# Optimization experiments

Measured on AMD Instinct MI355X. Metric: run time of the kernel, lower is better.

The kernel has to match this reference:

```python
import jax, jax.numpy as jnp
import numpy as np
from jax import lax

B, T, D_IN, H, OUT = 64, 500, 89, 512, 61


def setup_inputs() -> dict:
    key = jax.random.key(0)
    ks = jax.random.split(key, 12)
    s = lambda *sh: 1.0 / np.sqrt(sh[-1])
    inp = {
        "x": jax.random.normal(ks[0], (B, T, D_IN), dtype=jnp.float32),
        "lengths": jax.random.randint(ks[1], (B,), 1, T + 1, dtype=jnp.int64),
        # layer 0: input 89 -> 2H gates; layers 1,2: input 2H (bidirectional concat)
        "W0": jax.random.normal(ks[2], (2 * H, D_IN), dtype=jnp.float32) * s(2 * H, D_IN),
        "U0": jax.random.normal(ks[3], (2 * H, H), dtype=jnp.float32) * s(2 * H, H),
        "W1": jax.random.normal(ks[4], (2 * H, 2 * H), dtype=jnp.float32) * s(2 * H, 2 * H),
        "U1": jax.random.normal(ks[5], (2 * H, H), dtype=jnp.float32) * s(2 * H, H),
        "W2": jax.random.normal(ks[6], (2 * H, 2 * H), dtype=jnp.float32) * s(2 * H, 2 * H),
        "U2": jax.random.normal(ks[7], (2 * H, H), dtype=jnp.float32) * s(2 * H, H),
        "fc_w": jax.random.normal(ks[8], (OUT, 2 * H), dtype=jnp.float32) * s(OUT, 2 * H),
        "fc_b": jnp.zeros((OUT,), dtype=jnp.float32),
    }
    return inp


def _ligru_layer(x, W, U):
    """Bidirectional LiGRU layer (SpeechBrain flip-and-stack trick, shared weights).
    x: [B, T, D] -> [B, T, 2H]."""
    b = x.shape[0]
    x2 = jnp.concatenate([x, x[:, ::-1]], axis=0)            # [2B, T, D]
    w = jnp.einsum('btd,gd->btg', x2, W)                      # precompute input proj [2B, T, 2H]
    h0 = jnp.zeros((2 * b, H), x.dtype)

    def step(h, wt):
        g = wt + h @ U.T                                      # [2B, 2H]
        a, z = g[:, :H], jax.nn.sigmoid(g[:, H:])
        h = z * h + (1.0 - z) * jnp.tanh(a)
        return h, h

    _, hs = lax.scan(step, h0, jnp.swapaxes(w, 0, 1))         # [T, 2B, H]
    hs = jnp.swapaxes(hs, 0, 1)                               # [2B, T, H]
    fwd, bwd = hs[:b], hs[b:, ::-1]
    return jnp.concatenate([fwd, bwd], axis=-1)               # [B, T, 2H]


def reference(x, lengths, W0, U0, W1, U1, W2, U2, fc_w, fc_b):
    h = _ligru_layer(x, W0, U0)
    h = _ligru_layer(h, W1, U1)
    h = _ligru_layer(h, W2, U2)
    out = jnp.einsum('bth,oh->bto', h, fc_w) + fc_b           # [B, T, OUT]
    # valid-frame selection (the torch helper packs frames < lengths[i]); keep
    # static shape by masking invalid timesteps to zero instead of packing.
    mask = (jnp.arange(T)[None, :] < lengths[:, None]).astype(out.dtype)
    return out * mask[:, :, None]
```

## Files before the change

kernel.cpp:

```cpp
#include <hip/hip_runtime.h>
#include <hip/hip_bf16.h>
#include <stdint.h>


typedef __attribute__((ext_vector_type(8))) short bf16x8;
typedef __attribute__((ext_vector_type(4))) float f32x4;
typedef __attribute__((ext_vector_type(4))) unsigned short u16x4;

#define AS1 __attribute__((address_space(1)))
#define AS3 __attribute__((address_space(3)))
#define GLDS16(g, s)                                                           \
  __builtin_amdgcn_global_load_lds((const AS1 void*)(g), (AS3 void*)(s), 16, 0, 0)

__device__ __forceinline__ unsigned short f2bf(float f) {
  unsigned u = __builtin_bit_cast(unsigned, f);
  u += 0x7fffu + ((u >> 16) & 1u);
  return (unsigned short)(u >> 16);
}
__device__ __forceinline__ float bf2f(unsigned short s) {
  unsigned u = ((unsigned)s) << 16;
  return __builtin_bit_cast(float, u);
}

__global__ void k_f2b(unsigned short* __restrict__ dst, const float* __restrict__ src,
                      int dstCols, int srcStride, int srcOff, int copyCols) {
  long r = blockIdx.x;
  const float* s = src + r * (long)srcStride + srcOff;
  unsigned short* d = dst + r * (long)dstCols;
  for (int c = threadIdx.x; c < dstCols; c += blockDim.x)
    d[c] = (c < copyCols) ? f2bf(s[c]) : (unsigned short)0;
}

__global__ void k_init(int* __restrict__ bar, unsigned short* __restrict__ fcPad) {
  int t = threadIdx.x;
  for (int i = t; i < 3 * 1024; i += 256) bar[i] = 0;
  for (int i = t; i < 6 * 512; i += 256) fcPad[i] = 0;
}

template <int OUTBF>
__global__ __launch_bounds__(256, 2) void k_gemm(
    const unsigned short* __restrict__ A, const unsigned short* __restrict__ Bt,
    void* __restrict__ C, int K, int ldc) {
  __shared__ __align__(16) unsigned short As[128 * 32];
  __shared__ __align__(16) unsigned short Bs[128 * 32];
  const int tid = threadIdx.x;
  const int w = tid >> 6, l = tid & 63;
  const int wm = w >> 1, wn = w & 1;
  const int l15 = l & 15, l4 = l >> 4;
  const long m0 = (long)blockIdx.x * 128;
  const long n0 = (long)blockIdx.y * 128;
  const int lr = l >> 2, lk = (l & 3) * 8;

  f32x4 acc[4][4] = {};

  for (int k0 = 0; k0 < K; k0 += 32) {
    __syncthreads();
#pragma unroll
    for (int i = 0; i < 2; ++i) {
      const int ra = w * 32 + i * 16;
      const unsigned short* ga = A + (m0 + ra + lr) * K + k0 + lk;
      const unsigned short* gb = Bt + (n0 + ra + lr) * K + k0 + lk;
      GLDS16(ga, As + ra * 32);
      GLDS16(gb, Bs + ra * 32);
    }
    asm volatile("s_waitcnt vmcnt(0)" ::: "memory");
    __syncthreads();
    bf16x8 af[4], bfv[4];
#pragma unroll
    for (int mt = 0; mt < 4; ++mt)
      af[mt] = *(const bf16x8*)(As + (wm * 64 + mt * 16 + l15) * 32 + l4 * 8);
#pragma unroll
    for (int nt = 0; nt < 4; ++nt)
      bfv[nt] = *(const bf16x8*)(Bs + (wn * 64 + nt * 16 + l15) * 32 + l4 * 8);
#pragma unroll
    for (int mt = 0; mt < 4; ++mt)
#pragma unroll
      for (int nt = 0; nt < 4; ++nt)
        acc[mt][nt] =
            __builtin_amdgcn_mfma_f32_16x16x32_bf16(af[mt], bfv[nt], acc[mt][nt], 0, 0, 0);
  }
  const int rr = l4 * 4, cc = l15;
#pragma unroll
  for (int mt = 0; mt < 4; ++mt)
#pragma unroll
    for (int nt = 0; nt < 4; ++nt) {
      const long col = n0 + wn * 64 + nt * 16 + cc;
#pragma unroll
      for (int j = 0; j < 4; ++j) {
        const long row = m0 + wm * 64 + mt * 16 + rr + j;
        if (OUTBF)
          ((unsigned short*)C)[row * ldc + col] = f2bf(acc[mt][nt][j]);
        else
          ((float*)C)[row * ldc + col] = acc[mt][nt][j];
      }
    }
}

template <int PAIRED, bool FAST>
__device__ __forceinline__ void scan_body(
    const int rg, const int ws, const int l, const int l15, const int l4,
    const int pl, const bf16x8* Ua, const bf16x8* Uz,
    const unsigned short* __restrict__ PQ, unsigned short* __restrict__ hs,
    unsigned short* __restrict__ hx, int* __restrict__ rgflags,
    int* __restrict__ myflag) {
  float h_own[4] = {0.f, 0.f, 0.f, 0.f};
  const int gc = 16 * ws + 4 * l4;
  const int r = rg * 16 + l15;

  u16x4 ra1 = {0, 0, 0, 0}, rz1 = {0, 0, 0, 0};
  u16x4 ra2 = {0, 0, 0, 0}, rz2 = {0, 0, 0, 0};
  auto issuePQ = [&](int t) {
    if (PAIRED) {
      const long b1 = ((long)r * 500 + t) * 1024;
      const int r2i = (r + 64) & 127;
      const long b2 = ((long)r2i * 500 + (499 - t)) * 1024;
      ra1 = __builtin_nontemporal_load((const u16x4*)(PQ + b1 + gc));
      rz1 = __builtin_nontemporal_load((const u16x4*)(PQ + b1 + 512 + gc));
      ra2 = __builtin_nontemporal_load((const u16x4*)(PQ + b2 + gc));
      rz2 = __builtin_nontemporal_load((const u16x4*)(PQ + b2 + 512 + gc));
    } else {
      const int rr = (r < 64) ? r : r - 64;
      const int tt = (r < 64) ? t : 499 - t;
      const long b1 = ((long)rr * 500 + tt) * 1024;
      ra1 = __builtin_nontemporal_load((const u16x4*)(PQ + b1 + gc));
      rz1 = __builtin_nontemporal_load((const u16x4*)(PQ + b1 + 512 + gc));
    }
  };
  issuePQ(0);

  for (int t = 0; t < 500; ++t) {
    f32x4 a0 = {0.f, 0.f, 0.f, 0.f}, a1 = {0.f, 0.f, 0.f, 0.f};
    f32x4 z0 = {0.f, 0.f, 0.f, 0.f}, z1 = {0.f, 0.f, 0.f, 0.f};
    if (t > 0) {
      int spins = 0;
      for (;;) {
        int f = FAST ? __hip_atomic_load(rgflags + pl, __ATOMIC_RELAXED,
                                         __HIP_MEMORY_SCOPE_AGENT)
                     : __hip_atomic_load(rgflags + pl, __ATOMIC_ACQUIRE,
                                         __HIP_MEMORY_SCOPE_AGENT);
        if (__all(f >= t)) break;
        if (++spins > (1 << 20)) break;
      }
      asm volatile("" ::: "memory");
      const unsigned short* slotBase =
          hx + (((long)((t - 1) & 3) * 8 + rg) * 32) * 256;
      bf16x8 hv[16];
#pragma unroll
      for (int kt = 0; kt < 16; ++kt) {
        const unsigned short* p =
            slotBase + (2 * kt + (l4 >> 1)) * 256 + l15 * 16 + 8 * (l4 & 1);
        if (FAST)
          asm volatile("global_load_dwordx4 %0, %1, off sc0"
                       : "=v"(hv[kt]) : "v"(p));
        else
          asm volatile("global_load_dwordx4 %0, %1, off sc0 sc1"
                       : "=v"(hv[kt]) : "v"(p));
      }
      asm volatile("s_waitcnt vmcnt(0)" ::: "memory");
      __builtin_amdgcn_sched_barrier(0);
#pragma unroll
      for (int kt = 0; kt < 16; kt += 2) {
        a0 = __builtin_amdgcn_mfma_f32_16x16x32_bf16(Ua[kt], hv[kt], a0, 0, 0, 0);
        z0 = __builtin_amdgcn_mfma_f32_16x16x32_bf16(Uz[kt], hv[kt], z0, 0, 0, 0);
        a1 = __builtin_amdgcn_mfma_f32_16x16x32_bf16(Ua[kt + 1], hv[kt + 1], a1, 0, 0, 0);
        z1 = __builtin_amdgcn_mfma_f32_16x16x32_bf16(Uz[kt + 1], hv[kt + 1], z1, 0, 0, 0);
      }
    }
    u16x4 hv4;
#pragma unroll
    for (int j = 0; j < 4; ++j) {
      float A = a0[j] + a1[j] + bf2f(ra1[j]);
      float Z = z0[j] + z1[j] + bf2f(rz1[j]);
      if (PAIRED) {
        A += bf2f(ra2[j]);
        Z += bf2f(rz2[j]);
      }
      const float zs = 1.f / (1.f + __expf(-Z));
      const float e2 = __expf(-2.f * fabsf(A));
      const float th = copysignf((1.f - e2) / (1.f + e2), A);
      h_own[j] = zs * h_own[j] + (1.f - zs) * th;
      hv4[j] = f2bf(h_own[j]);
    }
    unsigned short* tile = hx + (((long)(t & 3) * 8 + rg) * 32 + ws) * 256;
    *(u16x4*)(tile + l15 * 16 + 4 * l4) = hv4;
    asm volatile("s_waitcnt vmcnt(0)" ::: "memory");
    if (!FAST) __threadfence();
    if (l == 0) {
      if (FAST)
        __hip_atomic_store(myflag, t + 1, __ATOMIC_RELAXED, __HIP_MEMORY_SCOPE_AGENT);
      else
        __hip_atomic_store(myflag, t + 1, __ATOMIC_RELEASE, __HIP_MEMORY_SCOPE_AGENT);
    }
    *(u16x4*)(hs + ((long)r * 500 + t) * 512 + gc) = hv4;
    if (t < 499) issuePQ(t + 1);
  }
}

template <int PAIRED>
__global__ __launch_bounds__(64, 1) void k_scan(
    const unsigned short* __restrict__ Ub,
    const unsigned short* __restrict__ PQ,
    unsigned short* __restrict__ hs,
    unsigned short* __restrict__ hx,
    int* __restrict__ flags,
    int* __restrict__ xcc) {
  const int bid = blockIdx.x;
  const int rg = bid & 7, ws = bid >> 3;
  const int l = threadIdx.x;
  const int l15 = l & 15, l4 = l >> 4, pl = l & 31;

  int myxcc;
  asm volatile("s_getreg_b32 %0, hwreg(HW_REG_XCC_ID)" : "=s"(myxcc));
  myxcc &= 0xff;
  if (l == 0)
    __hip_atomic_store(xcc + rg * 64 + ws, myxcc + 1, __ATOMIC_RELEASE,
                       __HIP_MEMORY_SCOPE_AGENT);

  bf16x8 Ua[16], Uz[16];
  {
    const int ja = 16 * ws + l15;
    const unsigned short* pa = Ub + ja * 512 + 8 * l4;
    const unsigned short* pz = pa + 512 * 512;
#pragma unroll
    for (int kt = 0; kt < 16; ++kt) {
      Ua[kt] = *(const bf16x8*)(pa + kt * 32);
      Uz[kt] = *(const bf16x8*)(pz + kt * 32);
    }
  }

  bool fast;
  {
    int v;
    for (;;) {
      v = __hip_atomic_load(xcc + rg * 64 + pl, __ATOMIC_ACQUIRE,
                            __HIP_MEMORY_SCOPE_AGENT);
      if (__all(v != 0)) break;
      __builtin_amdgcn_s_sleep(1);
    }
    fast = __all(v == myxcc + 1);
  }

  int* myflag = flags + rg * 64 + ws;
  int* rgflags = flags + rg * 64;
  if (fast)
    scan_body<PAIRED, true>(rg, ws, l, l15, l4, pl, Ua, Uz, PQ, hs, hx, rgflags, myflag);
  else
    scan_body<PAIRED, false>(rg, ws, l, l15, l4, pl, Ua, Uz, PQ, hs, hx, rgflags, myflag);
}

__global__ void k_combine(const float* __restrict__ Rf, const float* __restrict__ fcb,
                          const int* __restrict__ len32, float* __restrict__ out) {
  int i = blockIdx.x * 256 + threadIdx.x;
  if (i >= 64 * 500 * 61) return;
  const int o = i % 61;
  const int bt = i / 61;
  const int t = bt % 500;
  const int b = bt / 500;
  const bool is64 = (len32[1] == 0);
  const int L = is64 ? len32[2 * b] : len32[b];
  float v = 0.f;
  if (t < L) {
    v = Rf[((long)(b * 500 + t)) * 128 + o] +
        Rf[((long)((b + 64) * 500 + (499 - t))) * 128 + 61 + o] + fcb[o];
  }
  out[i] = v;
}

extern "C" void kernel_launch(void* const* d_in, const int* in_sizes, int n_in,
                              void* d_out, int out_size, void* d_ws, size_t ws_size,
                              hipStream_t stream) {
  (void)in_sizes; (void)n_in; (void)out_size; (void)ws_size;
  const float* x = (const float*)d_in[0];
  const int* len32 = (const int*)d_in[1];
  const float* W0 = (const float*)d_in[2];
  const float* U0 = (const float*)d_in[3];
  const float* W1 = (const float*)d_in[4];
  const float* U1 = (const float*)d_in[5];
  const float* W2 = (const float*)d_in[6];
  const float* U2 = (const float*)d_in[7];
  const float* fcw = (const float*)d_in[8];
  const float* fcb = (const float*)d_in[9];
  float* out = (float*)d_out;

  char* ws = (char*)d_ws;
  size_t off = 0;
  auto alloc = [&](size_t bytes) -> void* {
    void* p = ws + off;
    off = (off + bytes + 255) & ~(size_t)255;
    return p;
  };
  unsigned short* hs   = (unsigned short*)alloc(128ull * 500 * 512 * 2);
  unsigned short* PQ   = (unsigned short*)alloc(128ull * 500 * 1024 * 2);
  float*          Rf   = (float*)PQ;
  unsigned short* xb   = (unsigned short*)alloc(32000ull * 96 * 2);
  unsigned short* W0b  = (unsigned short*)alloc(1024ull * 96 * 2);
  unsigned short* WaT1 = (unsigned short*)alloc(1024ull * 512 * 2);
  unsigned short* WbT1 = (unsigned short*)alloc(1024ull * 512 * 2);
  unsigned short* WaT2 = (unsigned short*)alloc(1024ull * 512 * 2);
  unsigned short* WbT2 = (unsigned short*)alloc(1024ull * 512 * 2);
  unsigned short* Ub0  = (unsigned short*)alloc(1024ull * 512 * 2);
  unsigned short* Ub1  = (unsigned short*)alloc(1024ull * 512 * 2);
  unsigned short* Ub2  = (unsigned short*)alloc(1024ull * 512 * 2);
  unsigned short* fcT  = (unsigned short*)alloc(128ull * 512 * 2);
  unsigned short* hx   = (unsigned short*)alloc(4ull * 8 * 32 * 256 * 2);
  int*            bar  = (int*)alloc(3 * 1024 * 4);

  k_init<<<1, 256, 0, stream>>>(bar, fcT + 122 * 512);
  k_f2b<<<32000, 128, 0, stream>>>(xb, x, 96, 89, 0, 89);
  k_f2b<<<1024, 128, 0, stream>>>(W0b, W0, 96, 89, 0, 89);
  k_f2b<<<1024, 128, 0, stream>>>(WaT1, W1, 512, 1024, 0, 512);
  k_f2b<<<1024, 128, 0, stream>>>(WbT1, W1, 512, 1024, 512, 512);
  k_f2b<<<1024, 128, 0, stream>>>(WaT2, W2, 512, 1024, 0, 512);
  k_f2b<<<1024, 128, 0, stream>>>(WbT2, W2, 512, 1024, 512, 512);
  k_f2b<<<1024, 128, 0, stream>>>(Ub0, U0, 512, 512, 0, 512);
  k_f2b<<<1024, 128, 0, stream>>>(Ub1, U1, 512, 512, 0, 512);
  k_f2b<<<1024, 128, 0, stream>>>(Ub2, U2, 512, 512, 0, 512);
  k_f2b<<<61, 128, 0, stream>>>(fcT, fcw, 512, 1024, 0, 512);
  k_f2b<<<61, 128, 0, stream>>>(fcT + 61 * 512, fcw, 512, 1024, 512, 512);

  k_gemm<1><<<dim3(250, 8), 256, 0, stream>>>(xb, W0b, PQ, 96, 1024);
  k_scan<0><<<256, 64, 0, stream>>>(Ub0, PQ, hs, hx, bar + 0, bar + 512);
  k_gemm<1><<<dim3(250, 8), 256, 0, stream>>>(hs, WaT1, PQ, 512, 1024);
  k_gemm<1><<<dim3(250, 8), 256, 0, stream>>>(hs + 32000ull * 512, WbT1,
                                              PQ + 32000ull * 1024, 512, 1024);
  k_scan<1><<<256, 64, 0, stream>>>(Ub1, PQ, hs, hx, bar + 1024, bar + 1536);
  k_gemm<1><<<dim3(250, 8), 256, 0, stream>>>(hs, WaT2, PQ, 512, 1024);
  k_gemm<1><<<dim3(250, 8), 256, 0, stream>>>(hs + 32000ull * 512, WbT2,
                                              PQ + 32000ull * 1024, 512, 1024);
  k_scan<1><<<256, 64, 0, stream>>>(Ub2, PQ, hs, hx, bar + 2048, bar + 2560);
  k_gemm<0><<<dim3(500, 1), 256, 0, stream>>>(hs, fcT, Rf, 512, 128);
  k_combine<<<(64 * 500 * 61 + 255) / 256, 256, 0, stream>>>(Rf, fcb, len32, out);
}
```

Measured before the change: 3.101 ms.

## Hand-schedule scan step memory ops with SGPR bases, split waits, early partial store

Rewrites the recurrent scan inner loop to use inline-asm global loads and stores with scalar base pointers plus immediate offsets, cutting per-step 64-bit address arithmetic. In the fast path, the h-tile loads are split into two halves so the first half of the MFMAs can start after a partial vmcnt wait. The new h value is stored in two dword halves so the first store can issue before the second half of the gate math finishes. Correctness now depends on hand-coded byte offsets and on the inline-asm waitcnt ordering, which the compiler no longer checks.

```diff
diff --git a/kernel.cpp b/kernel.cpp
--- a/kernel.cpp
+++ b/kernel.cpp
@@ -6,6 +6,7 @@
 typedef __attribute__((ext_vector_type(8))) short bf16x8;
 typedef __attribute__((ext_vector_type(4))) float f32x4;
 typedef __attribute__((ext_vector_type(4))) unsigned short u16x4;
+typedef __attribute__((ext_vector_type(2))) unsigned int u32x2;
 
 #define AS1 __attribute__((address_space(1)))
 #define AS3 __attribute__((address_space(3)))
@@ -107,26 +108,48 @@
   const int gc = 16 * ws + 4 * l4;
   const int r = rg * 16 + l15;
 
+  const unsigned voffG0 = (unsigned)((l4 >> 1) * 512 + l15 * 32 + (l4 & 1) * 16);
+  const unsigned voffG1 = voffG0 + 4096u;
+  const unsigned voffG2 = voffG0 + 8192u;
+  const unsigned voffG3 = voffG0 + 12288u;
+  const unsigned voffT = (unsigned)(l15 * 32 + l4 * 8);
+  const unsigned long long hxB =
+      (unsigned long long)(uintptr_t)hx + (unsigned)(rg * 16384);
+
+  const int fwd1 = (PAIRED || rg < 4) ? 1 : 0;
+  const unsigned voffP1 =
+      (unsigned)(fwd1 ? r : r - 64) * 1024000u + (unsigned)(gc * 2);
+  unsigned long long sP1 =
+      (unsigned long long)(uintptr_t)PQ + (fwd1 ? 0u : 1021952u);
+  const long long dP1 = fwd1 ? 2048 : -2048;
+  const unsigned voffP2 =
+      (unsigned)((r + 64) & 127) * 1024000u + (unsigned)(gc * 2);
+  unsigned long long sP2 = (unsigned long long)(uintptr_t)PQ + 1021952u;
+  const unsigned voffH = (unsigned)r * 512000u + (unsigned)(gc * 2);
+  unsigned long long sH = (unsigned long long)(uintptr_t)hs;
+
   u16x4 ra1 = {0, 0, 0, 0}, rz1 = {0, 0, 0, 0};
   u16x4 ra2 = {0, 0, 0, 0}, rz2 = {0, 0, 0, 0};
-  auto issuePQ = [&](int t) {
-    if (PAIRED) {
-      const long b1 = ((long)r * 500 + t) * 1024;
-      const int r2i = (r + 64) & 127;
-      const long b2 = ((long)r2i * 500 + (499 - t)) * 1024;
-      ra1 = __builtin_nontemporal_load((const u16x4*)(PQ + b1 + gc));
-      rz1 = __builtin_nontemporal_load((const u16x4*)(PQ + b1 + 512 + gc));
-      ra2 = __builtin_nontemporal_load((const u16x4*)(PQ + b2 + gc));
-      rz2 = __builtin_nontemporal_load((const u16x4*)(PQ + b2 + 512 + gc));
-    } else {
-      const int rr = (r < 64) ? r : r - 64;
-      const int tt = (r < 64) ? t : 499 - t;
-      const long b1 = ((long)rr * 500 + tt) * 1024;
-      ra1 = __builtin_nontemporal_load((const u16x4*)(PQ + b1 + gc));
-      rz1 = __builtin_nontemporal_load((const u16x4*)(PQ + b1 + 512 + gc));
-    }
-  };
-  issuePQ(0);
+
+#define PQ_ISSUE()                                                             \
+  do {                                                                         \
+    asm volatile("global_load_dwordx2 %0, %1, %2 nt"                           \
+                 : "=v"(ra1) : "v"(voffP1), "s"(sP1));                         \
+    asm volatile("global_load_dwordx2 %0, %1, %2 offset:1024 nt"               \
+                 : "=v"(rz1) : "v"(voffP1), "s"(sP1));                         \
+    if (PAIRED) {                                                              \
+      asm volatile("global_load_dwordx2 %0, %1, %2 nt"                         \
+                   : "=v"(ra2) : "v"(voffP2), "s"(sP2));                       \
+      asm volatile("global_load_dwordx2 %0, %1, %2 offset:1024 nt"             \
+                   : "=v"(rz2) : "v"(voffP2), "s"(sP2));                       \
+    }                                                                          \
+  } while (0)
+
+  PQ_ISSUE();
+  sP1 += dP1;
+  sP2 -= 2048;
+  asm volatile("s_waitcnt vmcnt(0)" ::: "memory");
+  __builtin_amdgcn_sched_barrier(0);
 
   for (int t = 0; t < 500; ++t) {
     f32x4 a0 = {0.f, 0.f, 0.f, 0.f}, a1 = {0.f, 0.f, 0.f, 0.f};
@@ -142,33 +165,53 @@
         if (++spins > (1 << 20)) break;
       }
       asm volatile("" ::: "memory");
-      const unsigned short* slotBase =
-          hx + (((long)((t - 1) & 3) * 8 + rg) * 32) * 256;
+      const unsigned long long sbSlot =
+          hxB + (unsigned)(((t - 1) & 3) * 131072);
       bf16x8 hv[16];
-#pragma unroll
-      for (int kt = 0; kt < 16; ++kt) {
-        const unsigned short* p =
-            slotBase + (2 * kt + (l4 >> 1)) * 256 + l15 * 16 + 8 * (l4 & 1);
-        if (FAST)
-          asm volatile("global_load_dwordx4 %0, %1, off sc0"
-                       : "=v"(hv[kt]) : "v"(p));
-        else
-          asm volatile("global_load_dwordx4 %0, %1, off sc0 sc1"
-                       : "=v"(hv[kt]) : "v"(p));
-      }
-      asm volatile("s_waitcnt vmcnt(0)" ::: "memory");
+#define HLOAD(idx, vg, IMMSTR)                                                 \
+      do {                                                                     \
+        if (FAST)                                                              \
+          asm volatile("global_load_dwordx4 %0, %1, %2 offset:" IMMSTR " sc0"  \
+                       : "=v"(hv[idx]) : "v"(vg), "s"(sbSlot));                \
+        else                                                                   \
+          asm volatile("global_load_dwordx4 %0, %1, %2 offset:" IMMSTR         \
+                       " sc0 sc1"                                              \
+                       : "=v"(hv[idx]) : "v"(vg), "s"(sbSlot));                \
+      } while (0)
+      HLOAD(0, voffG0, "0");     HLOAD(1, voffG0, "1024");
+      HLOAD(2, voffG0, "2048");  HLOAD(3, voffG0, "3072");
+      HLOAD(4, voffG1, "0");     HLOAD(5, voffG1, "1024");
+      HLOAD(6, voffG1, "2048");  HLOAD(7, voffG1, "3072");
+      HLOAD(8, voffG2, "0");     HLOAD(9, voffG2, "1024");
+      HLOAD(10, voffG2, "2048"); HLOAD(11, voffG2, "3072");
+      HLOAD(12, voffG3, "0");    HLOAD(13, voffG3, "1024");
+      HLOAD(14, voffG3, "2048"); HLOAD(15, voffG3, "3072");
+#undef HLOAD
+      if (FAST)
+        asm volatile("s_waitcnt vmcnt(8)" ::: "memory");
+      else
+        asm volatile("s_waitcnt vmcnt(0)" ::: "memory");
       __builtin_amdgcn_sched_barrier(0);
 #pragma unroll
-      for (int kt = 0; kt < 16; kt += 2) {
+      for (int kt = 0; kt < 8; kt += 2) {
         a0 = __builtin_amdgcn_mfma_f32_16x16x32_bf16(Ua[kt], hv[kt], a0, 0, 0, 0);
         z0 = __builtin_amdgcn_mfma_f32_16x16x32_bf16(Uz[kt], hv[kt], z0, 0, 0, 0);
         a1 = __builtin_amdgcn_mfma_f32_16x16x32_bf16(Ua[kt + 1], hv[kt + 1], a1, 0, 0, 0);
         z1 = __builtin_amdgcn_mfma_f32_16x16x32_bf16(Uz[kt + 1], hv[kt + 1], z1, 0, 0, 0);
       }
-    }
-    u16x4 hv4;
-#pragma unroll
-    for (int j = 0; j < 4; ++j) {
+      if (FAST) {
+        asm volatile("s_waitcnt vmcnt(0)" ::: "memory");
+        __builtin_amdgcn_sched_barrier(0);
+      }
+#pragma unroll
+      for (int kt = 8; kt < 16; kt += 2) {
+        a0 = __builtin_amdgcn_mfma_f32_16x16x32_bf16(Ua[kt], hv[kt], a0, 0, 0, 0);
+        z0 = __builtin_amdgcn_mfma_f32_16x16x32_bf16(Uz[kt], hv[kt], z0, 0, 0, 0);
+        a1 = __builtin_amdgcn_mfma_f32_16x16x32_bf16(Ua[kt + 1], hv[kt + 1], a1, 0, 0, 0);
+        z1 = __builtin_amdgcn_mfma_f32_16x16x32_bf16(Uz[kt + 1], hv[kt + 1], z1, 0, 0, 0);
+      }
+    }
+    auto upd = [&](int j) {
       float A = a0[j] + a1[j] + bf2f(ra1[j]);
       float Z = z0[j] + z1[j] + bf2f(rz1[j]);
       if (PAIRED) {
@@ -179,21 +222,62 @@
       const float e2 = __expf(-2.f * fabsf(A));
       const float th = copysignf((1.f - e2) / (1.f + e2), A);
       h_own[j] = zs * h_own[j] + (1.f - zs) * th;
-      hv4[j] = f2bf(h_own[j]);
-    }
-    unsigned short* tile = hx + (((long)(t & 3) * 8 + rg) * 32 + ws) * 256;
-    *(u16x4*)(tile + l15 * 16 + 4 * l4) = hv4;
-    asm volatile("s_waitcnt vmcnt(0)" ::: "memory");
-    if (!FAST) __threadfence();
-    if (l == 0) {
-      if (FAST)
-        __hip_atomic_store(myflag, t + 1, __ATOMIC_RELAXED, __HIP_MEMORY_SCOPE_AGENT);
-      else
-        __hip_atomic_store(myflag, t + 1, __ATOMIC_RELEASE, __HIP_MEMORY_SCOPE_AGENT);
-    }
-    *(u16x4*)(hs + ((long)r * 500 + t) * 512 + gc) = hv4;
-    if (t < 499) issuePQ(t + 1);
+    };
+    const unsigned long long sT =
+        hxB + (unsigned)((t & 3) * 131072 + ws * 512);
+    upd(0);
+    upd(1);
+    const unsigned d01 =
+        (unsigned)f2bf(h_own[0]) | ((unsigned)f2bf(h_own[1]) << 16);
+    if (FAST) {
+      asm volatile("global_store_dword %0, %1, %2"
+                   :: "v"(voffT), "v"(d01), "s"(sT) : "memory");
+    }
+    upd(2);
+    upd(3);
+    const unsigned d23 =
+        (unsigned)f2bf(h_own[2]) | ((unsigned)f2bf(h_own[3]) << 16);
+    if (FAST) {
+      asm volatile("global_store_dword %0, %1, %2 offset:4"
+                   :: "v"(voffT), "v"(d23), "s"(sT) : "memory");
+      asm volatile("s_waitcnt vmcnt(0)" ::: "memory");
+      __builtin_amdgcn_sched_barrier(0);
+      if (l == 0)
+        __hip_atomic_store(myflag, t + 1, __ATOMIC_RELAXED,
+                           __HIP_MEMORY_SCOPE_AGENT);
+      {
+        u32x2 hd2;
+        hd2[0] = d01;
+        hd2[1] = d23;
+        asm volatile("global_store_dwordx2 %0, %1, %2"
+                     :: "v"(voffH), "v"(hd2), "s"(sH) : "memory");
+      }
+      if (t < 499) PQ_ISSUE();
+    } else {
+      u32x2 hd;
+      hd[0] = d01;
+      hd[1] = d23;
+      asm volatile("global_store_dwordx2 %0, %1, %2"
+                   :: "v"(voffT), "v"(hd), "s"(sT) : "memory");
+      asm volatile("s_waitcnt vmcnt(0)" ::: "memory");
+      __threadfence();
+      if (l == 0)
+        __hip_atomic_store(myflag, t + 1, __ATOMIC_RELEASE,
+                           __HIP_MEMORY_SCOPE_AGENT);
+      {
+        u32x2 hd2;
+        hd2[0] = d01;
+        hd2[1] = d23;
+        asm volatile("global_store_dwordx2 %0, %1, %2"
+                     :: "v"(voffH), "v"(hd2), "s"(sH) : "memory");
+      }
+      if (t < 499) PQ_ISSUE();
+    }
+    sH += 1024;
+    sP1 += dP1;
+    sP2 -= 2048;
   }
+#undef PQ_ISSUE
 }
 
 template <int PAIRED>
```

Measured after the change: 3.137 ms. Within noise of the previous version (+1.2%).
